# Kernel tuning notes

Hardware: AMD Instinct MI355X
Metric: run time of the kernel (lower is better)

The kernel has to match this reference:

```python
import jax, jax.numpy as jnp
import numpy as np

K_TOP = 2  # top-k experts per token


def setup_inputs() -> dict:
    key = jax.random.key(0)
    k1, k2, k3 = jax.random.split(key, 3)
    B, S, H, E = 4, 2048, 1024, 8
    hidden_states = jax.random.normal(k1, (B, S, H), dtype=jnp.float32)
    router_w = jax.random.normal(k2, (E, H), dtype=jnp.float32) * 0.02
    expert_weights = jax.random.normal(k3, (E, H, H), dtype=jnp.float32) * 0.02
    return {"hidden_states": hidden_states, "router_w": router_w, "expert_weights": expert_weights}


def reference(hidden_states, router_w, expert_weights):
    B, S, H = hidden_states.shape
    x = hidden_states.reshape(-1, H)                      # [N, H], N = B*S
    logits = x @ router_w.T                               # [N, E]
    probs = jax.nn.softmax(logits, axis=-1)               # [N, E]
    topk_vals, topk_idx = jax.lax.top_k(probs, K_TOP)     # [N, K]
    topk_w = topk_vals / (topk_vals.sum(-1, keepdims=True) + 1e-6)  # [N, K]

    # Dense per-expert GEMM over all tokens (single-device dispatch = identity)
    expert_out = jnp.einsum('nh,eho->eno', x, expert_weights)  # [E, N, H]

    # all_to_all_combine: gather each token's K expert outputs
    combined = jnp.take_along_axis(
        expert_out.transpose(1, 0, 2),                    # [N, E, H]
        topk_idx[:, :, None], axis=1)                     # [N, K, H]
    combined = combined.transpose(1, 0, 2)                # [K, N, H]

    # remap bias: sum over last dim of one-hot(topk_idx) * router_prob == gathered prob
    remap_bias = jnp.take_along_axis(probs, topk_idx, axis=1).T[:, :, None]  # [K, N, 1]

    weights = topk_w.T[:, :, None]                        # [K, N, 1]
    out = ((combined + remap_bias) * weights).sum(axis=0) # [N, H]
    return out.reshape(B, S, H)
```

## Files before the change

### kernel.cpp

```cpp
#include <hip/hip_runtime.h>
#include <hip/hip_fp16.h>
#include <cstdint>

typedef unsigned short u16;
typedef __attribute__((ext_vector_type(8))) short short8;
typedef __attribute__((ext_vector_type(4))) float float4v;

#define NTOK 8192
#define HDIM 1024
#define NEXP 8
#define TM 128
#define TN 128
#define BK 32
#define NITER (HDIM / BK)
#define LA_N (TM * BK)
#define LB_N (TN * BK)
#define MAXT 136
#define WBLK 8192
#define RBLK 2048

__device__ __forceinline__ u16 f2bf(float f) {
    union { float f; uint32_t u; } v; v.f = f;
    uint32_t u = v.u;
    return (u16)((u + 0x7FFFu + ((u >> 16) & 1u)) >> 16);
}

__device__ __forceinline__ void gll16(const u16* g, u16* l) {
    __builtin_amdgcn_global_load_lds(
        (const __attribute__((address_space(1))) uint32_t*)g,
        (__attribute__((address_space(3))) uint32_t*)l,
        16, 0, 0);
}

__global__ __launch_bounds__(256) void prep(const float* __restrict__ x,
                                            const float* __restrict__ rw,
                                            const float* __restrict__ ew,
                                            u16* __restrict__ x_bf,
                                            u16* __restrict__ w_bf,
                                            float* __restrict__ wt0,
                                            float* __restrict__ wt1,
                                            float* __restrict__ biasv,
                                            int* __restrict__ sel,
                                            int* __restrict__ ctrl) {
    if (blockIdx.x == 0 && threadIdx.x < 132) ctrl[threadIdx.x] = 0;

    if (blockIdx.x < WBLK) {
        __shared__ float tile[32][33];
        const int bid = blockIdx.x;
        const int e  = bid >> 10;
        const int k0 = (bid & 31) * 32;
        const int n0 = ((bid >> 5) & 31) * 32;
        const int r = threadIdx.x >> 3;
        const int c = (threadIdx.x & 7) * 4;
        const float4 v = *(const float4*)(ew + ((size_t)e << 20) + (size_t)(k0 + r) * HDIM + n0 + c);
        tile[r][c] = v.x; tile[r][c+1] = v.y; tile[r][c+2] = v.z; tile[r][c+3] = v.w;
        __syncthreads();
        ushort4 o;
        o.x = f2bf(tile[c][r]); o.y = f2bf(tile[c+1][r]);
        o.z = f2bf(tile[c+2][r]); o.w = f2bf(tile[c+3][r]);
        *(ushort4*)(w_bf + ((size_t)e << 20) + (size_t)(n0 + r) * HDIM + k0 + c) = o;
    } else {
        const int wv = threadIdx.x >> 6;
        const int l  = threadIdx.x & 63;
        const int n  = (blockIdx.x - WBLK) * 4 + wv;
        const float4* xr = (const float4*)(x + (size_t)n * HDIM);
        ushort4* xo = (ushort4*)(x_bf + (size_t)n * HDIM);

        float4 xv[4];
#pragma unroll
        for (int t = 0; t < 4; t++) {
            xv[t] = xr[t * 64 + l];
            ushort4 p;
            p.x = f2bf(xv[t].x); p.y = f2bf(xv[t].y);
            p.z = f2bf(xv[t].z); p.w = f2bf(xv[t].w);
            xo[t * 64 + l] = p;
        }

        float logits[NEXP];
#pragma unroll
        for (int e = 0; e < NEXP; e++) {
            const float4* rwe = (const float4*)(rw + e * HDIM);
            float acc = 0.f;
#pragma unroll
            for (int t = 0; t < 4; t++) {
                const float4 r = rwe[t * 64 + l];
                acc += xv[t].x * r.x + xv[t].y * r.y + xv[t].z * r.z + xv[t].w * r.w;
            }
#pragma unroll
            for (int s = 32; s > 0; s >>= 1) acc += __shfl_xor(acc, s, 64);
            logits[e] = acc;
        }

        if (l == 0) {
            float mx = logits[0];
#pragma unroll
            for (int e = 1; e < NEXP; e++) mx = fmaxf(mx, logits[e]);
            float p[NEXP]; float sum = 0.f;
#pragma unroll
            for (int e = 0; e < NEXP; e++) { p[e] = expf(logits[e] - mx); sum += p[e]; }
            const float inv = 1.f / sum;
#pragma unroll
            for (int e = 0; e < NEXP; e++) p[e] *= inv;
            int e0 = 0;
#pragma unroll
            for (int e = 1; e < NEXP; e++) if (p[e] > p[e0]) e0 = e;
            int e1 = (e0 == 0) ? 1 : 0;
#pragma unroll
            for (int e = 0; e < NEXP; e++) if (e != e0 && p[e] > p[e1]) e1 = e;
            const float p0 = p[e0], p1 = p[e1];
            const float wsum = p0 + p1 + 1e-6f;
            const float w0 = p0 / wsum, w1 = p1 / wsum;
            wt0[n] = w0; wt1[n] = w1;
            biasv[n] = w0 * p0 + w1 * p1;
            sel[n] = e0 | (e1 << 8);
        }
    }
}

__global__ __launch_bounds__(256) void build_lists(const int* __restrict__ sel,
                                                   int* __restrict__ lists,
                                                   int* __restrict__ ctrl,
                                                   int* __restrict__ tmap) {
    const int n  = blockIdx.x * 256 + threadIdx.x;
    const int wv = threadIdx.x >> 6;
    const int l  = threadIdx.x & 63;
    const int s  = sel[n];
    const int e0 = s & 0xFF, e1 = s >> 8;
    __shared__ int wcnt[NEXP][4];
    __shared__ int ebase[NEXP];
    int pf0 = 0, pf1 = 0;
    const unsigned long long ltmask = (1ULL << l) - 1ULL;
#pragma unroll
    for (int e = 0; e < NEXP; e++) {
        const int slot = (e0 == e) ? 0 : ((e1 == e) ? 1 : -1);
        const unsigned long long bal = __ballot(slot >= 0);
        const int pf = __popcll(bal & ltmask);
        if (slot == 0) pf0 = pf;
        if (slot == 1) pf1 = pf;
        if (l == 0) wcnt[e][wv] = __popcll(bal);
    }
    __syncthreads();
    if (threadIdx.x < NEXP) {
        const int e = threadIdx.x;
        const int tot = wcnt[e][0] + wcnt[e][1] + wcnt[e][2] + wcnt[e][3];
        ebase[e] = atomicAdd(&ctrl[e * 16], tot);
    }
    __syncthreads();
    int off0 = ebase[e0], off1 = ebase[e1];
#pragma unroll
    for (int i = 0; i < 4; i++) {
        off0 += (i < wv) ? wcnt[e0][i] : 0;
        off1 += (i < wv) ? wcnt[e1][i] : 0;
    }
    lists[e0 * NTOK + off0 + pf0] = n;
    lists[e1 * NTOK + off1 + pf1] = n | 0x10000;

    __shared__ int lastflag;
    __threadfence();
    if (threadIdx.x == 0) lastflag = (atomicAdd(&ctrl[128], 1) == (int)gridDim.x - 1);
    __syncthreads();
    if (lastflag) {
        __shared__ int tbase[NEXP + 1];
        if (threadIdx.x == 0) {
            int acc = 0;
            for (int e = 0; e < NEXP; e++) {
                tbase[e] = acc;
                acc += (atomicAdd(&ctrl[e * 16], 0) + TM - 1) / TM;
            }
            tbase[NEXP] = acc;
        }
        __syncthreads();
        for (int i = threadIdx.x; i < MAXT; i += 256) {
            int v = -1;
#pragma unroll
            for (int e = 0; e < NEXP; e++)
                if (i >= tbase[e] && i < tbase[e + 1]) v = (e << 16) | (i - tbase[e]);
            tmap[i] = v;
        }
    }
}

__global__ __launch_bounds__(256, 3) void moe_gemm(const u16* __restrict__ x_bf,
                                                   const u16* __restrict__ wt_bf,
                                                   const int* __restrict__ lists,
                                                   const int* __restrict__ ctrl,
                                                   const int* __restrict__ tmap,
                                                   const float* __restrict__ wt0,
                                                   const float* __restrict__ wt1,
                                                   const float* __restrict__ biasv,
                                                   __half* __restrict__ stage0,
                                                   __half* __restrict__ stage1) {
    const int ent = tmap[blockIdx.x];
    if (ent < 0) return;
    const int e = ent >> 16;
    const int tile_m = (ent & 0xFFFF) * TM;
    const int cnt = ctrl[e * 16];
    const int tn = blockIdx.y * TN;

    __shared__ u16 lA[3 * LA_N];
    __shared__ u16 lB[3 * LB_N];
    __shared__ int   toks[TM];
    __shared__ float wgt[TM];
    __shared__ float bia[TM];
    __shared__ int   slt[TM];

    const int t  = threadIdx.x;
    const int wv = t >> 6;
    const int l  = t & 63;

    if (t < TM) {
        const int idx = tile_m + t;
        int tok = 0; float w = 0.f, b = 0.f; int sl = 0;
        if (idx < cnt) {
            const int entry = lists[e * NTOK + idx];
            tok = entry & 0xFFFF;
            sl = entry >> 16;
            w = sl ? wt1[tok] : wt0[tok];
            b = sl ? 0.f : biasv[tok];
        }
        toks[t] = tok; wgt[t] = w; bia[t] = b; slt[t] = sl;
    }
    __syncthreads();

    const u16* gA[2]; const u16* gB[2]; int dAB[2];
#pragma unroll
    for (int i = 0; i < 2; i++) {
        const int slot = (i * 4 + wv) * 64 + l;
        const int row  = slot >> 2;
        const int c    = (slot & 3) ^ ((row >> 1) & 3);
        gA[i] = x_bf + (size_t)toks[row] * HDIM + c * 8;
        gB[i] = wt_bf + ((size_t)e << 20) + (size_t)(tn + row) * HDIM + c * 8;
        dAB[i] = (i * 4 + wv) * 512;
    }

    const int wm = (wv & 1) * 64;
    const int wn = (wv >> 1) * 64;
    const int fm = l & 15;
    const int fq = l >> 4;
    int aoff[4], boff[4];
#pragma unroll
    for (int i = 0; i < 4; i++) {
        const int ra = wm + i * 16 + fm;
        const int rb = wn + i * 16 + fm;
        aoff[i] = ra * BK + ((fq ^ ((ra >> 1) & 3)) * 8);
        boff[i] = rb * BK + ((fq ^ ((rb >> 1) & 3)) * 8);
    }

    float4v acc[4][4];
#pragma unroll
    for (int i = 0; i < 4; i++)
#pragma unroll
        for (int j = 0; j < 4; j++) { float4v z = {0.f, 0.f, 0.f, 0.f}; acc[i][j] = z; }

    short8 afr[2][4], bfr[2][4];

#pragma unroll
    for (int tk = 0; tk < 3; tk++) {
#pragma unroll
        for (int i = 0; i < 2; i++) {
            gll16(gA[i] + tk * BK, lA + tk * LA_N + dAB[i]);
            gll16(gB[i] + tk * BK, lB + tk * LB_N + dAB[i]);
        }
    }
    asm volatile("s_waitcnt vmcnt(8)\n\ts_barrier" ::: "memory");
#pragma unroll
    for (int i = 0; i < 4; i++) {
        afr[0][i] = *(const short8*)&lA[aoff[i]];
        bfr[0][i] = *(const short8*)&lB[boff[i]];
    }

#pragma unroll
    for (int it = 0; it < NITER; ++it) {
        const int cs = it & 1;
        const int ns = cs ^ 1;

        if (it == 0) {
            asm volatile("s_waitcnt vmcnt(4)\n\ts_barrier" ::: "memory");
        } else if (it < NITER - 1) {
            asm volatile("s_waitcnt vmcnt(0)\n\ts_barrier" ::: "memory");
        }

        if (it >= 1 && it + 2 < NITER) {
            const int nb = (it + 2) % 3;
            const int nk = (it + 2) * BK;
#pragma unroll
            for (int i = 0; i < 2; i++) {
                gll16(gA[i] + nk, lA + nb * LA_N + dAB[i]);
                gll16(gB[i] + nk, lB + nb * LB_N + dAB[i]);
            }
        }

        if (it + 1 < NITER) {
            const u16* ca = lA + ((it + 1) % 3) * LA_N;
            const u16* cb = lB + ((it + 1) % 3) * LB_N;
#pragma unroll
            for (int i = 0; i < 4; i++) {
                afr[ns][i] = *(const short8*)&ca[aoff[i]];
                bfr[ns][i] = *(const short8*)&cb[boff[i]];
            }
            asm volatile("s_waitcnt lgkmcnt(8)" ::: "memory");
        } else {
            asm volatile("s_waitcnt lgkmcnt(0)" ::: "memory");
        }
        __builtin_amdgcn_sched_barrier(0);

        __builtin_amdgcn_s_setprio(1);
#pragma unroll
        for (int i = 0; i < 4; i++)
#pragma unroll
            for (int nf = 0; nf < 4; nf++)
                acc[i][nf] = __builtin_amdgcn_mfma_f32_16x16x32_bf16(
                    afr[cs][i], bfr[cs][nf], acc[i][nf], 0, 0, 0);
        __builtin_amdgcn_s_setprio(0);
    }

#pragma unroll
    for (int mf = 0; mf < 4; mf++) {
#pragma unroll
        for (int r = 0; r < 4; r++) {
            const int m_local = wm + mf * 16 + fq * 4 + r;
            if (tile_m + m_local < cnt) {
                const int tok = toks[m_local];
                const float w = wgt[m_local], b = bia[m_local];
                __half* sp = (slt[m_local] ? stage1 : stage0) + (size_t)tok * HDIM;
#pragma unroll
                for (int nf = 0; nf < 4; nf++) {
                    const int h = tn + wn + nf * 16 + fm;
                    sp[h] = __float2half(acc[mf][nf][r] * w + b);
                }
            }
        }
    }
}

__global__ __launch_bounds__(256) void combine(const __half* __restrict__ s0,
                                               const __half* __restrict__ s1,
                                               float* __restrict__ out) {
    const size_t idx = ((size_t)blockIdx.x * 256 + threadIdx.x) * 8;
    union { uint4 v; __half h[8]; } a, b;
    a.v = *(const uint4*)(s0 + idx);
    b.v = *(const uint4*)(s1 + idx);
    float4 o0, o1;
    o0.x = __half2float(a.h[0]) + __half2float(b.h[0]);
    o0.y = __half2float(a.h[1]) + __half2float(b.h[1]);
    o0.z = __half2float(a.h[2]) + __half2float(b.h[2]);
    o0.w = __half2float(a.h[3]) + __half2float(b.h[3]);
    o1.x = __half2float(a.h[4]) + __half2float(b.h[4]);
    o1.y = __half2float(a.h[5]) + __half2float(b.h[5]);
    o1.z = __half2float(a.h[6]) + __half2float(b.h[6]);
    o1.w = __half2float(a.h[7]) + __half2float(b.h[7]);
    *(float4*)(out + idx)     = o0;
    *(float4*)(out + idx + 4) = o1;
}

extern "C" void kernel_launch(void* const* d_in, const int* in_sizes, int n_in,
                              void* d_out, int out_size, void* d_ws, size_t ws_size,
                              hipStream_t stream) {
    const float* x  = (const float*)d_in[0];
    const float* rw = (const float*)d_in[1];
    const float* ew = (const float*)d_in[2];
    float* out = (float*)d_out;

    char* ws = (char*)d_ws;
    u16*    x_bf   = (u16*)ws;
    u16*    w_bf   = (u16*)(ws + 16777216);
    __half* stage0 = (__half*)(ws + 33554432);
    __half* stage1 = (__half*)(ws + 50331648);
    float*  wt0    = (float*)(ws + 67108864);
    float*  wt1    = (float*)(ws + 67141632);
    float*  biasv  = (float*)(ws + 67174400);
    int*    sel    = (int*)(ws + 67207168);
    int*    lists  = (int*)(ws + 67239936);
    int*    ctrl   = (int*)(ws + 67502080);
    int*    tmap   = (int*)(ws + 67502720);

    prep<<<WBLK + RBLK, 256, 0, stream>>>(x, rw, ew, x_bf, w_bf, wt0, wt1, biasv, sel, ctrl);
    build_lists<<<NTOK / 256, 256, 0, stream>>>(sel, lists, ctrl, tmap);
    moe_gemm<<<dim3(MAXT, HDIM / TN, 1), 256, 0, stream>>>(
        x_bf, w_bf, lists, ctrl, tmap, wt0, wt1, biasv, stage0, stage1);
    combine<<<(NTOK * HDIM) / (256 * 8), 256, 0, stream>>>(stage0, stage1, out);
}
```

Before: 196.1 us.

## Load MFMA fragments directly from global memory, dropping LDS staging

```diff
diff --git a/kernel.cpp b/kernel.cpp
--- a/kernel.cpp
+++ b/kernel.cpp
@@ -13,8 +13,6 @@
 #define TN 128
 #define BK 32
 #define NITER (HDIM / BK)
-#define LA_N (TM * BK)
-#define LB_N (TN * BK)
 #define MAXT 136
 #define WBLK 8192
 #define RBLK 2048
@@ -23,13 +21,6 @@
     union { float f; uint32_t u; } v; v.f = f;
     uint32_t u = v.u;
     return (u16)((u + 0x7FFFu + ((u >> 16) & 1u)) >> 16);
-}
-
-__device__ __forceinline__ void gll16(const u16* g, u16* l) {
-    __builtin_amdgcn_global_load_lds(
-        (const __attribute__((address_space(1))) uint32_t*)g,
-        (__attribute__((address_space(3))) uint32_t*)l,
-        16, 0, 0);
 }
 
 __global__ __launch_bounds__(256) void prep(const float* __restrict__ x,
@@ -197,8 +188,6 @@
     const int cnt = ctrl[e * 16];
     const int tn = blockIdx.y * TN;
 
-    __shared__ u16 lA[3 * LA_N];
-    __shared__ u16 lB[3 * LB_N];
     __shared__ int   toks[TM];
     __shared__ float wgt[TM];
     __shared__ float bia[TM];
@@ -222,28 +211,19 @@
     }
     __syncthreads();
 
-    const u16* gA[2]; const u16* gB[2]; int dAB[2];
-#pragma unroll
-    for (int i = 0; i < 2; i++) {
-        const int slot = (i * 4 + wv) * 64 + l;
-        const int row  = slot >> 2;
-        const int c    = (slot & 3) ^ ((row >> 1) & 3);
-        gA[i] = x_bf + (size_t)toks[row] * HDIM + c * 8;
-        gB[i] = wt_bf + ((size_t)e << 20) + (size_t)(tn + row) * HDIM + c * 8;
-        dAB[i] = (i * 4 + wv) * 512;
-    }
-
     const int wm = (wv & 1) * 64;
     const int wn = (wv >> 1) * 64;
     const int fm = l & 15;
     const int fq = l >> 4;
-    int aoff[4], boff[4];
+
+    const u16* const wbase = wt_bf + ((size_t)e << 20);
+    uint32_t oA[4], oB[4];
 #pragma unroll
     for (int i = 0; i < 4; i++) {
         const int ra = wm + i * 16 + fm;
-        const int rb = wn + i * 16 + fm;
-        aoff[i] = ra * BK + ((fq ^ ((ra >> 1) & 3)) * 8);
-        boff[i] = rb * BK + ((fq ^ ((rb >> 1) & 3)) * 8);
+        oA[i] = (uint32_t)toks[ra] * HDIM + fq * 8;
+        const int rb = tn + wn + i * 16 + fm;
+        oB[i] = (uint32_t)rb * HDIM + fq * 8;
     }
 
     float4v acc[4][4];
@@ -255,18 +235,9 @@
     short8 afr[2][4], bfr[2][4];
 
 #pragma unroll
-    for (int tk = 0; tk < 3; tk++) {
-#pragma unroll
-        for (int i = 0; i < 2; i++) {
-            gll16(gA[i] + tk * BK, lA + tk * LA_N + dAB[i]);
-            gll16(gB[i] + tk * BK, lB + tk * LB_N + dAB[i]);
-        }
-    }
-    asm volatile("s_waitcnt vmcnt(8)\n\ts_barrier" ::: "memory");
-#pragma unroll
     for (int i = 0; i < 4; i++) {
-        afr[0][i] = *(const short8*)&lA[aoff[i]];
-        bfr[0][i] = *(const short8*)&lB[boff[i]];
+        afr[0][i] = *(const short8*)(x_bf + oA[i]);
+        bfr[0][i] = *(const short8*)(wbase + oB[i]);
     }
 
 #pragma unroll
@@ -274,35 +245,14 @@
         const int cs = it & 1;
         const int ns = cs ^ 1;
 
-        if (it == 0) {
-            asm volatile("s_waitcnt vmcnt(4)\n\ts_barrier" ::: "memory");
-        } else if (it < NITER - 1) {
-            asm volatile("s_waitcnt vmcnt(0)\n\ts_barrier" ::: "memory");
-        }
-
-        if (it >= 1 && it + 2 < NITER) {
-            const int nb = (it + 2) % 3;
-            const int nk = (it + 2) * BK;
-#pragma unroll
-            for (int i = 0; i < 2; i++) {
-                gll16(gA[i] + nk, lA + nb * LA_N + dAB[i]);
-                gll16(gB[i] + nk, lB + nb * LB_N + dAB[i]);
+        if (it + 1 < NITER) {
+            const int nk = (it + 1) * BK;
+#pragma unroll
+            for (int i = 0; i < 4; i++) {
+                afr[ns][i] = *(const short8*)(x_bf + oA[i] + nk);
+                bfr[ns][i] = *(const short8*)(wbase + oB[i] + nk);
             }
         }
-
-        if (it + 1 < NITER) {
-            const u16* ca = lA + ((it + 1) % 3) * LA_N;
-            const u16* cb = lB + ((it + 1) % 3) * LB_N;
-#pragma unroll
-            for (int i = 0; i < 4; i++) {
-                afr[ns][i] = *(const short8*)&ca[aoff[i]];
-                bfr[ns][i] = *(const short8*)&cb[boff[i]];
-            }
-            asm volatile("s_waitcnt lgkmcnt(8)" ::: "memory");
-        } else {
-            asm volatile("s_waitcnt lgkmcnt(0)" ::: "memory");
-        }
-        __builtin_amdgcn_sched_barrier(0);
 
         __builtin_amdgcn_s_setprio(1);
 #pragma unroll
```

Result: slower. 286.7 us (+46.2%).

## Split-K the expert GEMM and combine via fp32 atomics into output

Applied to the files above, without the earlier changes.

```diff
diff --git a/kernel.cpp b/kernel.cpp
--- a/kernel.cpp
+++ b/kernel.cpp
@@ -12,7 +12,8 @@
 #define TM 128
 #define TN 128
 #define BK 32
-#define NITER (HDIM / BK)
+#define KSPL 2
+#define NITER (HDIM / BK / KSPL)
 #define LA_N (TM * BK)
 #define LB_N (TN * BK)
 #define MAXT 136
@@ -41,10 +42,16 @@
                                             float* __restrict__ wt1,
                                             float* __restrict__ biasv,
                                             int* __restrict__ sel,
-                                            int* __restrict__ ctrl) {
+                                            int* __restrict__ ctrl,
+                                            float* __restrict__ out) {
     if (blockIdx.x == 0 && threadIdx.x < 132) ctrl[threadIdx.x] = 0;
 
     if (blockIdx.x < WBLK) {
+        {
+            const size_t zi = ((size_t)blockIdx.x * 256 + threadIdx.x) * 4;
+            float4 z; z.x = 0.f; z.y = 0.f; z.z = 0.f; z.w = 0.f;
+            *(float4*)(out + zi) = z;
+        }
         __shared__ float tile[32][33];
         const int bid = blockIdx.x;
         const int e  = bid >> 10;
@@ -188,21 +195,20 @@
                                                    const float* __restrict__ wt0,
                                                    const float* __restrict__ wt1,
                                                    const float* __restrict__ biasv,
-                                                   __half* __restrict__ stage0,
-                                                   __half* __restrict__ stage1) {
+                                                   float* __restrict__ out) {
     const int ent = tmap[blockIdx.x];
     if (ent < 0) return;
     const int e = ent >> 16;
     const int tile_m = (ent & 0xFFFF) * TM;
     const int cnt = ctrl[e * 16];
     const int tn = blockIdx.y * TN;
+    const int kz = blockIdx.z * (HDIM / KSPL);
 
     __shared__ u16 lA[3 * LA_N];
     __shared__ u16 lB[3 * LB_N];
     __shared__ int   toks[TM];
     __shared__ float wgt[TM];
     __shared__ float bia[TM];
-    __shared__ int   slt[TM];
 
     const int t  = threadIdx.x;
     const int wv = t >> 6;
@@ -210,15 +216,15 @@
 
     if (t < TM) {
         const int idx = tile_m + t;
-        int tok = 0; float w = 0.f, b = 0.f; int sl = 0;
+        int tok = 0; float w = 0.f, b = 0.f;
         if (idx < cnt) {
             const int entry = lists[e * NTOK + idx];
             tok = entry & 0xFFFF;
-            sl = entry >> 16;
+            const int sl = entry >> 16;
             w = sl ? wt1[tok] : wt0[tok];
-            b = sl ? 0.f : biasv[tok];
-        }
-        toks[t] = tok; wgt[t] = w; bia[t] = b; slt[t] = sl;
+            b = (sl || blockIdx.z) ? 0.f : biasv[tok];
+        }
+        toks[t] = tok; wgt[t] = w; bia[t] = b;
     }
     __syncthreads();
 
@@ -228,8 +234,8 @@
         const int slot = (i * 4 + wv) * 64 + l;
         const int row  = slot >> 2;
         const int c    = (slot & 3) ^ ((row >> 1) & 3);
-        gA[i] = x_bf + (size_t)toks[row] * HDIM + c * 8;
-        gB[i] = wt_bf + ((size_t)e << 20) + (size_t)(tn + row) * HDIM + c * 8;
+        gA[i] = x_bf + (size_t)toks[row] * HDIM + kz + c * 8;
+        gB[i] = wt_bf + ((size_t)e << 20) + (size_t)(tn + row) * HDIM + kz + c * 8;
         dAB[i] = (i * 4 + wv) * 512;
     }
 
@@ -322,35 +328,15 @@
             if (tile_m + m_local < cnt) {
                 const int tok = toks[m_local];
                 const float w = wgt[m_local], b = bia[m_local];
-                __half* sp = (slt[m_local] ? stage1 : stage0) + (size_t)tok * HDIM;
+                float* op = out + (size_t)tok * HDIM;
 #pragma unroll
                 for (int nf = 0; nf < 4; nf++) {
                     const int h = tn + wn + nf * 16 + fm;
-                    sp[h] = __float2half(acc[mf][nf][r] * w + b);
+                    atomicAdd(op + h, acc[mf][nf][r] * w + b);
                 }
             }
         }
     }
-}
-
-__global__ __launch_bounds__(256) void combine(const __half* __restrict__ s0,
-                                               const __half* __restrict__ s1,
-                                               float* __restrict__ out) {
-    const size_t idx = ((size_t)blockIdx.x * 256 + threadIdx.x) * 8;
-    union { uint4 v; __half h[8]; } a, b;
-    a.v = *(const uint4*)(s0 + idx);
-    b.v = *(const uint4*)(s1 + idx);
-    float4 o0, o1;
-    o0.x = __half2float(a.h[0]) + __half2float(b.h[0]);
-    o0.y = __half2float(a.h[1]) + __half2float(b.h[1]);
-    o0.z = __half2float(a.h[2]) + __half2float(b.h[2]);
-    o0.w = __half2float(a.h[3]) + __half2float(b.h[3]);
-    o1.x = __half2float(a.h[4]) + __half2float(b.h[4]);
-    o1.y = __half2float(a.h[5]) + __half2float(b.h[5]);
-    o1.z = __half2float(a.h[6]) + __half2float(b.h[6]);
-    o1.w = __half2float(a.h[7]) + __half2float(b.h[7]);
-    *(float4*)(out + idx)     = o0;
-    *(float4*)(out + idx + 4) = o1;
 }
 
 extern "C" void kernel_launch(void* const* d_in, const int* in_sizes, int n_in,
@@ -364,8 +350,6 @@
     char* ws = (char*)d_ws;
     u16*    x_bf   = (u16*)ws;
     u16*    w_bf   = (u16*)(ws + 16777216);
-    __half* stage0 = (__half*)(ws + 33554432);
-    __half* stage1 = (__half*)(ws + 50331648);
     float*  wt0    = (float*)(ws + 67108864);
     float*  wt1    = (float*)(ws + 67141632);
     float*  biasv  = (float*)(ws + 67174400);
@@ -374,9 +358,8 @@
     int*    ctrl   = (int*)(ws + 67502080);
     int*    tmap   = (int*)(ws + 67502720);
 
-    prep<<<WBLK + RBLK, 256, 0, stream>>>(x, rw, ew, x_bf, w_bf, wt0, wt1, biasv, sel, ctrl);
+    prep<<<WBLK + RBLK, 256, 0, stream>>>(x, rw, ew, x_bf, w_bf, wt0, wt1, biasv, sel, ctrl, out);
     build_lists<<<NTOK / 256, 256, 0, stream>>>(sel, lists, ctrl, tmap);
-    moe_gemm<<<dim3(MAXT, HDIM / TN, 1), 256, 0, stream>>>(
-        x_bf, w_bf, lists, ctrl, tmap, wt0, wt1, biasv, stage0, stage1);
-    combine<<<(NTOK * HDIM) / (256 * 8), 256, 0, stream>>>(stage0, stage1, out);
-}
+    moe_gemm<<<dim3(MAXT, HDIM / TN, KSPL), 256, 0, stream>>>(
+        x_bf, w_bf, lists, ctrl, tmap, wt0, wt1, biasv, out);
+}
```

New measurement: 254.2 us. +29.7%, slower.
